# Kernel tuning notes

Measured on AMD Instinct MI355X. Metric: run time of the kernel, lower is better.

## Reference

```python
import jax, jax.numpy as jnp
import numpy as np

N_NODES = 100000
N_EDGES = 600000
F_IN = 128
F_OUT = 128


def setup_inputs() -> dict:
    key = jax.random.key(0)
    ks = jax.random.split(key, 9)
    stdv = 1.0 / np.sqrt(F_OUT)
    return {
        "x": jax.random.normal(ks[0], (N_NODES, F_IN), dtype=jnp.float32),
        "weight": jax.random.uniform(ks[1], (F_IN, F_OUT), dtype=jnp.float32, minval=-stdv, maxval=stdv),
        "bias": jax.random.uniform(ks[2], (F_OUT,), dtype=jnp.float32, minval=-stdv, maxval=stdv),
        "vals0": jax.random.uniform(ks[3], (N_EDGES,), dtype=jnp.float32),
        "vals1": jax.random.uniform(ks[4], (N_EDGES,), dtype=jnp.float32),
        "rows0": jax.random.randint(ks[5], (N_EDGES,), 0, N_NODES, dtype=jnp.int32),
        "cols0": jax.random.randint(ks[6], (N_EDGES,), 0, N_NODES, dtype=jnp.int32),
        "rows1": jax.random.randint(ks[7], (N_EDGES,), 0, N_NODES, dtype=jnp.int32),
        "cols1": jax.random.randint(ks[8], (N_EDGES,), 0, N_NODES, dtype=jnp.int32),
    }


def _spmm(rows, cols, vals, dense, n):
    # COO sparse [n,n] @ dense [n,f]: gather source rows, scale, scatter-add to dest rows
    msgs = dense[cols] * vals[:, None]          # [E, f]
    return jax.ops.segment_sum(msgs, rows, num_segments=n)


def reference(x, weight, bias, vals0, vals1, rows0, cols0, rows1, cols1):
    n = x.shape[0]
    support = x @ weight                         # [N, F_OUT] dense GEMM
    out = _spmm(rows0, cols0, vals0, support, n) \
        + _spmm(rows1, cols1, vals1, support, n)
    return out + bias
```

## Files before the change

kernel.cpp:

```cpp
#include <hip/hip_runtime.h>


#define FDIM 128

typedef __attribute__((ext_vector_type(8))) short short8;
typedef __attribute__((ext_vector_type(4))) float floatx4;

__device__ __forceinline__ unsigned short f32_to_bf16(float f) {
    unsigned int u = __float_as_uint(f);
    unsigned int r = u + 0x7fffu + ((u >> 16) & 1u);
    return (unsigned short)(r >> 16);
}

__device__ __forceinline__ float bf16_lo(unsigned int u) {
    return __uint_as_float((u & 0xffffu) << 16);
}
__device__ __forceinline__ float bf16_hi(unsigned int u) {
    return __uint_as_float(u & 0xffff0000u);
}

__global__ __launch_bounds__(256) void wt_conv(const float* __restrict__ w,
                                               unsigned short* __restrict__ wt) {
    int idx = blockIdx.x * 256 + threadIdx.x;
    int nn = idx >> 7, k = idx & 127;
    wt[idx] = f32_to_bf16(w[(size_t)k * FDIM + nn]);
}

__global__ __launch_bounds__(256) void gemm_mfma(const float* __restrict__ x,
                                                 const unsigned short* __restrict__ wt,
                                                 unsigned short* __restrict__ support,
                                                 int n) {
    __shared__ __align__(16) short As[64][136];
    __shared__ __align__(16) short Bs[128][136];
    const int tid = threadIdx.x;
    const int m0 = blockIdx.x * 64;

    #pragma unroll
    for (int i = 0; i < 8; ++i) {
        int idx = tid + i * 256;
        int r = idx >> 5, c4 = idx & 31;
        float4 v = make_float4(0.f, 0.f, 0.f, 0.f);
        if (m0 + r < n) v = *(const float4*)(x + (size_t)(m0 + r) * FDIM + c4 * 4);
        short4 s;
        s.x = (short)f32_to_bf16(v.x); s.y = (short)f32_to_bf16(v.y);
        s.z = (short)f32_to_bf16(v.z); s.w = (short)f32_to_bf16(v.w);
        *(short4*)&As[r][c4 * 4] = s;
    }
    #pragma unroll
    for (int i = 0; i < 8; ++i) {
        int idx = tid + i * 256;
        int r = idx >> 4, c8 = idx & 15;
        short8 v = *(const short8*)(wt + (size_t)r * FDIM + c8 * 8);
        *(short8*)&Bs[r][c8 * 8] = v;
    }
    __syncthreads();

    const int wv = tid >> 6;
    const int lane = tid & 63;
    const int quad = lane >> 4;
    const int lr = lane & 15;

    floatx4 acc[8];
    #pragma unroll
    for (int nt = 0; nt < 8; ++nt) acc[nt] = (floatx4)0.f;

    #pragma unroll
    for (int ks = 0; ks < 4; ++ks) {
        short8 a = *(const short8*)&As[wv * 16 + lr][ks * 32 + quad * 8];
        #pragma unroll
        for (int nt = 0; nt < 8; ++nt) {
            short8 b = *(const short8*)&Bs[nt * 16 + lr][ks * 32 + quad * 8];
            acc[nt] = __builtin_amdgcn_mfma_f32_16x16x32_bf16(a, b, acc[nt], 0, 0, 0);
        }
    }

    #pragma unroll
    for (int i = 0; i < 4; ++i) {
        int row = m0 + wv * 16 + quad * 4 + i;
        if (row < n) {
            #pragma unroll
            for (int nt = 0; nt < 8; ++nt)
                support[(size_t)row * FDIM + nt * 16 + lr] = f32_to_bf16(acc[nt][i]);
        }
    }
}

__global__ __launch_bounds__(256) void hist_rows(const int* __restrict__ rows0,
                                                 const int* __restrict__ rows1,
                                                 int* __restrict__ count, int E) {
    int gid = blockIdx.x * 256 + threadIdx.x;
    if (gid >= 2 * E) return;
    int r = (gid < E) ? rows0[gid] : rows1[gid - E];
    atomicAdd(&count[r], 1);
}

__device__ __forceinline__ int block_incl_scan(int v, int tid, int* lds) {
    int lane = tid & 63, wv = tid >> 6;
    #pragma unroll
    for (int d = 1; d < 64; d <<= 1) {
        int y = __shfl_up(v, d);
        if (lane >= d) v += y;
    }
    if (lane == 63) lds[wv] = v;
    __syncthreads();
    if (wv == 0 && lane < 4) {
        int s = lds[lane];
        #pragma unroll
        for (int d = 1; d < 4; d <<= 1) {
            int y = __shfl_up(s, d);
            if (lane >= d) s += y;
        }
        lds[4 + lane] = s;
    }
    __syncthreads();
    int add = (wv > 0) ? lds[4 + wv - 1] : 0;
    return v + add;
}

__global__ __launch_bounds__(256) void block_sum(const int* __restrict__ count,
                                                 int* __restrict__ bsum, int n) {
    __shared__ int lds[8];
    int tid = threadIdx.x;
    int idx = blockIdx.x * 256 + tid;
    int v = (idx < n) ? count[idx] : 0;
    int inc = block_incl_scan(v, tid, lds);
    if (tid == 255) bsum[blockIdx.x] = inc;
}

__global__ __launch_bounds__(256) void scan_bsum(int* __restrict__ bsum, int nb) {
    __shared__ int lds[8];
    __shared__ int carry;
    int tid = threadIdx.x;
    if (tid == 0) carry = 0;
    __syncthreads();
    for (int base = 0; base < nb; base += 256) {
        int i = base + tid;
        int v = (i < nb) ? bsum[i] : 0;
        int inc = block_incl_scan(v, tid, lds);
        int c = carry;
        if (i < nb) bsum[i] = c + inc - v;
        __syncthreads();
        if (tid == 255) carry = c + inc;
        __syncthreads();
    }
}

__global__ __launch_bounds__(256) void write_ptr(const int* __restrict__ count,
                                                 const int* __restrict__ bscan,
                                                 int* __restrict__ rowptr,
                                                 int* __restrict__ cursor,
                                                 int n, int total) {
    __shared__ int lds[8];
    int tid = threadIdx.x;
    int idx = blockIdx.x * 256 + tid;
    int v = (idx < n) ? count[idx] : 0;
    int inc = block_incl_scan(v, tid, lds);
    if (idx < n) {
        int p = bscan[blockIdx.x] + inc - v;
        rowptr[idx] = p;
        cursor[idx] = p;
    }
    if (idx == 0) rowptr[n] = total;
}

__global__ __launch_bounds__(256) void scatter_rec(const int* __restrict__ rows0,
                                                   const int* __restrict__ cols0,
                                                   const float* __restrict__ vals0,
                                                   const int* __restrict__ rows1,
                                                   const int* __restrict__ cols1,
                                                   const float* __restrict__ vals1,
                                                   int* __restrict__ cursor,
                                                   int2* __restrict__ rec, int E) {
    int gid = blockIdx.x * 256 + threadIdx.x;
    if (gid >= 2 * E) return;
    int r, c; float v;
    if (gid < E) { r = rows0[gid]; c = cols0[gid]; v = vals0[gid]; }
    else         { int e = gid - E; r = rows1[e]; c = cols1[e]; v = vals1[e]; }
    int pos = atomicAdd(&cursor[r], 1);
    rec[pos] = make_int2(c, __float_as_int(v));
}

__global__ __launch_bounds__(256) void pull_csr(const unsigned short* __restrict__ support,
                                                const int* __restrict__ rowptr,
                                                const int2* __restrict__ rec,
                                                const float* __restrict__ bias,
                                                float* __restrict__ out, int n) {
    int wid = (blockIdx.x * 256 + threadIdx.x) >> 6;
    int lane = threadIdx.x & 63;
    if (wid >= n) return;
    int beg = rowptr[wid], end = rowptr[wid + 1];
    float ax = 0.f, ay = 0.f;
    const char* sp = (const char*)support;
    const unsigned loff = (unsigned)lane << 2;

    for (int base = beg; base < end; base += 64) {
        int m = end - base; if (m > 64) m = 64;
        long long pk = 0;
        if (lane < m) pk = *(const long long*)&rec[base + lane];
        int j = 0;
        for (; j + 4 <= m; j += 4) {
            long long p0 = __shfl(pk, j);
            long long p1 = __shfl(pk, j + 1);
            long long p2 = __shfl(pk, j + 2);
            long long p3 = __shfl(pk, j + 3);
            unsigned u0 = *(const unsigned*)(sp + (((unsigned)p0) << 8) + loff);
            unsigned u1 = *(const unsigned*)(sp + (((unsigned)p1) << 8) + loff);
            unsigned u2 = *(const unsigned*)(sp + (((unsigned)p2) << 8) + loff);
            unsigned u3 = *(const unsigned*)(sp + (((unsigned)p3) << 8) + loff);
            float v0 = __int_as_float((int)(p0 >> 32));
            float v1 = __int_as_float((int)(p1 >> 32));
            float v2 = __int_as_float((int)(p2 >> 32));
            float v3 = __int_as_float((int)(p3 >> 32));
            ax += v0 * bf16_lo(u0); ay += v0 * bf16_hi(u0);
            ax += v1 * bf16_lo(u1); ay += v1 * bf16_hi(u1);
            ax += v2 * bf16_lo(u2); ay += v2 * bf16_hi(u2);
            ax += v3 * bf16_lo(u3); ay += v3 * bf16_hi(u3);
        }
        for (; j < m; ++j) {
            long long p = __shfl(pk, j);
            unsigned u = *(const unsigned*)(sp + (((unsigned)p) << 8) + loff);
            float v = __int_as_float((int)(p >> 32));
            ax += v * bf16_lo(u); ay += v * bf16_hi(u);
        }
    }
    float2 b = *(const float2*)(bias + lane * 2);
    *(float2*)(out + (size_t)wid * FDIM + lane * 2) = make_float2(ax + b.x, ay + b.y);
}

__global__ __launch_bounds__(256) void init_bias(const float* __restrict__ bias,
                                                 float* __restrict__ out, int n) {
    int idx = blockIdx.x * 256 + threadIdx.x;
    int total = n * (FDIM / 4);
    if (idx < total) {
        int j = (idx & (FDIM / 4 - 1)) * 4;
        float4 b = *(const float4*)(bias + j);
        *(float4*)(out + (size_t)idx * 4) = b;
    }
}

__global__ __launch_bounds__(256) void scatter_bf16(
    const unsigned short* __restrict__ support,
    const int* __restrict__ rows0, const int* __restrict__ cols0, const float* __restrict__ vals0,
    const int* __restrict__ rows1, const int* __restrict__ cols1, const float* __restrict__ vals1,
    float* __restrict__ out, int E) {
    int gid = blockIdx.x * 256 + threadIdx.x;
    int lane = gid & 63;
    int eg = gid >> 6;
    if (eg >= 2 * E) return;
    int r, c; float v;
    if (eg < E) { r = rows0[eg]; c = cols0[eg]; v = vals0[eg]; }
    else        { int e = eg - E; r = rows1[e]; c = cols1[e]; v = vals1[e]; }
    unsigned int u = *(const unsigned int*)(support + (size_t)c * FDIM + lane * 2);
    float sx = bf16_lo(u);
    float sy = bf16_hi(u);
    float* op = out + (size_t)r * FDIM + lane * 2;
    atomicAdd(op,     sx * v);
    atomicAdd(op + 1, sy * v);
}

static inline size_t align256(size_t v) { return (v + 255) & ~(size_t)255; }

extern "C" void kernel_launch(void* const* d_in, const int* in_sizes, int n_in,
                              void* d_out, int out_size, void* d_ws, size_t ws_size,
                              hipStream_t stream) {
    const float* x     = (const float*)d_in[0];
    const float* w     = (const float*)d_in[1];
    const float* bias  = (const float*)d_in[2];
    const float* vals0 = (const float*)d_in[3];
    const float* vals1 = (const float*)d_in[4];
    const int*   rows0 = (const int*)d_in[5];
    const int*   cols0 = (const int*)d_in[6];
    const int*   rows1 = (const int*)d_in[7];
    const int*   cols1 = (const int*)d_in[8];
    const int n = in_sizes[0] / FDIM;
    const int E = in_sizes[3];
    float* out = (float*)d_out;

    const int NB = (n + 255) / 256;

    size_t off = 0;
    unsigned short* support = (unsigned short*)((char*)d_ws + off);
    off = align256(off + (size_t)n * FDIM * 2);
    unsigned short* wt = (unsigned short*)((char*)d_ws + off);
    off = align256(off + (size_t)FDIM * FDIM * 2);
    int*  count  = (int*)((char*)d_ws + off);  off = align256(off + (size_t)n * 4);
    int*  rowptr = (int*)((char*)d_ws + off);  off = align256(off + (size_t)(n + 1) * 4);
    int*  cursor = (int*)((char*)d_ws + off);  off = align256(off + (size_t)n * 4);
    int*  bsum   = (int*)((char*)d_ws + off);  off = align256(off + (size_t)NB * 4);
    int2* rec    = (int2*)((char*)d_ws + off); off = align256(off + (size_t)2 * E * 8);

    wt_conv<<<(FDIM * FDIM) / 256, 256, 0, stream>>>(w, wt);
    gemm_mfma<<<(n + 63) / 64, 256, 0, stream>>>(x, wt, support, n);

    if (off <= ws_size) {
        hipMemsetAsync(count, 0, (size_t)n * 4, stream);
        int eb = (2 * E + 255) / 256;
        hist_rows<<<eb, 256, 0, stream>>>(rows0, rows1, count, E);
        block_sum<<<NB, 256, 0, stream>>>(count, bsum, n);
        scan_bsum<<<1, 256, 0, stream>>>(bsum, NB);
        write_ptr<<<NB, 256, 0, stream>>>(count, bsum, rowptr, cursor, n, 2 * E);
        scatter_rec<<<eb, 256, 0, stream>>>(rows0, cols0, vals0, rows1, cols1, vals1,
                                            cursor, rec, E);
        pull_csr<<<(n + 3) / 4, 256, 0, stream>>>(support, rowptr, rec, bias, out, n);
    } else {
        int total4 = n * (FDIM / 4);
        init_bias<<<(total4 + 255) / 256, 256, 0, stream>>>(bias, out, n);
        long long tthreads = 2LL * E * 64;
        int blocks = (int)((tthreads + 255) / 256);
        scatter_bf16<<<blocks, 256, 0, stream>>>(support, rows0, cols0, vals0,
                                                 rows1, cols1, vals1, out, E);
    }
}
```

Before: 325.8 us.

## Record atomic rank in histogram and partition CSR scatter by row range

Measured after the change: 278.2 us. 14.6% less time.

```diff
diff --git a/kernel.cpp b/kernel.cpp
--- a/kernel.cpp
+++ b/kernel.cpp
@@ -2,6 +2,7 @@
 
 
 #define FDIM 128
+#define EPB 2048
 
 typedef __attribute__((ext_vector_type(8))) short short8;
 typedef __attribute__((ext_vector_type(4))) float floatx4;
@@ -87,11 +88,12 @@
 
 __global__ __launch_bounds__(256) void hist_rows(const int* __restrict__ rows0,
                                                  const int* __restrict__ rows1,
-                                                 int* __restrict__ count, int E) {
+                                                 int* __restrict__ count,
+                                                 int* __restrict__ rank, int E) {
     int gid = blockIdx.x * 256 + threadIdx.x;
     if (gid >= 2 * E) return;
     int r = (gid < E) ? rows0[gid] : rows1[gid - E];
-    atomicAdd(&count[r], 1);
+    rank[gid] = atomicAdd(&count[r], 1);
 }
 
 __device__ __forceinline__ int block_incl_scan(int v, int tid, int* lds) {
@@ -148,36 +150,38 @@
 __global__ __launch_bounds__(256) void write_ptr(const int* __restrict__ count,
                                                  const int* __restrict__ bscan,
                                                  int* __restrict__ rowptr,
-                                                 int* __restrict__ cursor,
                                                  int n, int total) {
     __shared__ int lds[8];
     int tid = threadIdx.x;
     int idx = blockIdx.x * 256 + tid;
     int v = (idx < n) ? count[idx] : 0;
     int inc = block_incl_scan(v, tid, lds);
-    if (idx < n) {
-        int p = bscan[blockIdx.x] + inc - v;
-        rowptr[idx] = p;
-        cursor[idx] = p;
-    }
+    if (idx < n) rowptr[idx] = bscan[blockIdx.x] + inc - v;
     if (idx == 0) rowptr[n] = total;
 }
 
-__global__ __launch_bounds__(256) void scatter_rec(const int* __restrict__ rows0,
-                                                   const int* __restrict__ cols0,
-                                                   const float* __restrict__ vals0,
-                                                   const int* __restrict__ rows1,
-                                                   const int* __restrict__ cols1,
-                                                   const float* __restrict__ vals1,
-                                                   int* __restrict__ cursor,
-                                                   int2* __restrict__ rec, int E) {
-    int gid = blockIdx.x * 256 + threadIdx.x;
-    if (gid >= 2 * E) return;
-    int r, c; float v;
-    if (gid < E) { r = rows0[gid]; c = cols0[gid]; v = vals0[gid]; }
-    else         { int e = gid - E; r = rows1[e]; c = cols1[e]; v = vals1[e]; }
-    int pos = atomicAdd(&cursor[r], 1);
-    rec[pos] = make_int2(c, __float_as_int(v));
+__global__ __launch_bounds__(256) void scatter_part(
+    const int* __restrict__ rows0, const int* __restrict__ cols0, const float* __restrict__ vals0,
+    const int* __restrict__ rows1, const int* __restrict__ cols1, const float* __restrict__ vals1,
+    const int* __restrict__ rank, const int* __restrict__ rowptr,
+    int2* __restrict__ rec, int E, int nper) {
+    const int p = blockIdx.x & 7;
+    const int base = (blockIdx.x >> 3) * EPB;
+    const int tid = threadIdx.x;
+    #pragma unroll
+    for (int it = 0; it < EPB / 256; ++it) {
+        int gid = base + it * 256 + tid;
+        if (gid < 2 * E) {
+            int r = (gid < E) ? rows0[gid] : rows1[gid - E];
+            if (r / nper == p) {
+                int c; float v;
+                if (gid < E) { c = cols0[gid]; v = vals0[gid]; }
+                else         { int e = gid - E; c = cols1[e]; v = vals1[e]; }
+                int pos = rowptr[r] + rank[gid];
+                rec[pos] = make_int2(c, __float_as_int(v));
+            }
+        }
+    }
 }
 
 __global__ __launch_bounds__(256) void pull_csr(const unsigned short* __restrict__ support,
@@ -285,7 +289,7 @@
     off = align256(off + (size_t)FDIM * FDIM * 2);
     int*  count  = (int*)((char*)d_ws + off);  off = align256(off + (size_t)n * 4);
     int*  rowptr = (int*)((char*)d_ws + off);  off = align256(off + (size_t)(n + 1) * 4);
-    int*  cursor = (int*)((char*)d_ws + off);  off = align256(off + (size_t)n * 4);
+    int*  rank   = (int*)((char*)d_ws + off);  off = align256(off + (size_t)2 * E * 4);
     int*  bsum   = (int*)((char*)d_ws + off);  off = align256(off + (size_t)NB * 4);
     int2* rec    = (int2*)((char*)d_ws + off); off = align256(off + (size_t)2 * E * 8);
 
@@ -295,12 +299,15 @@
     if (off <= ws_size) {
         hipMemsetAsync(count, 0, (size_t)n * 4, stream);
         int eb = (2 * E + 255) / 256;
-        hist_rows<<<eb, 256, 0, stream>>>(rows0, rows1, count, E);
+        hist_rows<<<eb, 256, 0, stream>>>(rows0, rows1, count, rank, E);
         block_sum<<<NB, 256, 0, stream>>>(count, bsum, n);
         scan_bsum<<<1, 256, 0, stream>>>(bsum, NB);
-        write_ptr<<<NB, 256, 0, stream>>>(count, bsum, rowptr, cursor, n, 2 * E);
-        scatter_rec<<<eb, 256, 0, stream>>>(rows0, cols0, vals0, rows1, cols1, vals1,
-                                            cursor, rec, E);
+        write_ptr<<<NB, 256, 0, stream>>>(count, bsum, rowptr, n, 2 * E);
+        int nper = (n + 7) / 8;
+        int ntiles = (2 * E + EPB - 1) / EPB;
+        scatter_part<<<ntiles * 8, 256, 0, stream>>>(rows0, cols0, vals0,
+                                                     rows1, cols1, vals1,
+                                                     rank, rowptr, rec, E, nper);
         pull_csr<<<(n + 3) / 4, 256, 0, stream>>>(support, rowptr, rec, bias, out, n);
     } else {
         int total4 = n * (FDIM / 4);
```
